# Kernel tuning notes

Measured on AMD Instinct MI355X. Metric: run time of the kernel, lower is better.

The kernel has to match this reference:

```python
import jax, jax.numpy as jnp
import numpy as np

H = 4                      # num_heads hard-coded in SDHGNN
NAMES = ["self", "cross", "self", "cross"]
POOL_SIZES = [2, 2, 2, 2]
MIN_NGHS = 128             # minium_nghs
EPS = 1e-3                 # InstanceNorm1d eps


def _pw(x, W, b):
    # pointwise Conv1d(kernel=1): [B, Cin, N] -> [B, Cout, N]
    return jnp.einsum('oi,bin->bon', W, x) + b[None, :, None]


def _instnorm(x):
    # InstanceNorm1d (no affine): normalize over N per (B, C)
    m = jnp.mean(x, axis=2, keepdims=True)
    v = jnp.mean((x - m) ** 2, axis=2, keepdims=True)
    return (x - m) * jax.lax.rsqrt(v + EPS)


def _attn_prop(x, src, p):
    # SharedAttentionalPropagation (sharing_attention=False):
    # MultiHeadedAttention + concat + MLP residual update.
    Wq, bq, Wk, bk, Wv, bv, Wm, bm, W1, b1, W2, b2 = p
    B, D, N = x.shape
    dh = D // H
    q = _pw(x, Wq, bq).reshape(B, dh, H, N)
    k = _pw(src, Wk, bk).reshape(B, dh, H, -1)
    v = _pw(src, Wv, bv).reshape(B, dh, H, -1)
    scores = jnp.einsum('bdhn,bdhm->bhnm', q, k) * (dh ** -0.5)
    prob = jax.nn.softmax(scores, axis=-1)                     # [B,H,N,M]
    msg = jnp.einsum('bhnm,bdhm->bdhn', prob, v).reshape(B, D, N)
    msg = _pw(msg, Wm, bm)
    y = jnp.concatenate([x, msg], axis=1)                      # [B,2D,N]
    h = jax.nn.relu(_instnorm(_pw(y, W1, b1)))
    return x + _pw(h, W2, b2), prob


def _gather(x, idx):
    # x: [B,D,N], idx: [B,K] -> [B,D,K]
    return jnp.take_along_axis(
        x, jnp.broadcast_to(idx[:, None, :], (x.shape[0], x.shape[1], idx.shape[1])), axis=2)


def _pool(prob, idx, pool_size):
    # pooling_by_prob (4-D prob branch): mean over heads, sum over queries,
    # top-k by importance, sorted indices, gather global indexes.
    K = idx.shape[1]
    p = prob.mean(axis=1).sum(axis=1)                          # [B,K]
    k = min(max(K // pool_size, MIN_NGHS), K)
    _, top = jax.lax.top_k(p, k)
    top = jnp.sort(top, axis=1)
    return jnp.take_along_axis(idx, top, axis=1)


def setup_inputs() -> dict:
    key = jax.random.key(0)
    B, D, N, L = 2, 128, 2048, 4
    ks = jax.random.split(key, 16)
    s = lambda fan: 1.0 / np.sqrt(fan)
    inp = {
        'x0': jax.random.normal(ks[0], (B, D, N), jnp.float32),
        'x1': jax.random.normal(ks[1], (B, D, N), jnp.float32),
        'Wq': jax.random.normal(ks[2], (L, D, D), jnp.float32) * s(D),
        'bq': jax.random.normal(ks[3], (L, D), jnp.float32) * 0.01,
        'Wk': jax.random.normal(ks[4], (L, D, D), jnp.float32) * s(D),
        'bk': jax.random.normal(ks[5], (L, D), jnp.float32) * 0.01,
        'Wv': jax.random.normal(ks[6], (L, D, D), jnp.float32) * s(D),
        'bv': jax.random.normal(ks[7], (L, D), jnp.float32) * 0.01,
        'Wm': jax.random.normal(ks[8], (L, D, D), jnp.float32) * s(D),
        'bm': jax.random.normal(ks[9], (L, D), jnp.float32) * 0.01,
        'W1': jax.random.normal(ks[10], (L, 2 * D, 2 * D), jnp.float32) * s(2 * D),
        'b1': jax.random.normal(ks[11], (L, 2 * D), jnp.float32) * 0.01,
        'W2': jax.random.normal(ks[12], (L, D, 2 * D), jnp.float32) * s(2 * D),
        'b2': jnp.zeros((L, D), jnp.float32),  # nn.init.constant_(mlp[-1].bias, 0)
    }
    return inp


def reference(x0, x1, Wq, bq, Wk, bk, Wv, bv, Wm, bm, W1, b1, W2, b2):
    B, D, N = x0.shape
    idx0 = jnp.broadcast_to(jnp.arange(N, dtype=jnp.int32)[None], (B, N))
    idx1 = idx0
    for l, (name, ps) in enumerate(zip(NAMES, POOL_SIZES)):
        p = (Wq[l], bq[l], Wk[l], bk[l], Wv[l], bv[l],
             Wm[l], bm[l], W1[l], b1[l], W2[l], b2[l])
        if name == 'self':
            s0, s1 = _gather(x0, idx0), _gather(x1, idx1)
        else:
            s0, s1 = _gather(x1, idx1), _gather(x0, idx0)
        x0, prob0 = _attn_prop(x0, s0, p)
        x1, prob1 = _attn_prop(x1, s1, p)
        if name == 'self':
            idx0 = _pool(prob0, idx0, ps)
            idx1 = _pool(prob1, idx1, ps)
        else:
            idx1 = _pool(prob0, idx1, ps)
            idx0 = _pool(prob1, idx0, ps)
    return jnp.stack([x0, x1], axis=0)   # [2, B, D, N]
```

## Files before the change

kernel.cpp:

```cpp
#include <hip/hip_runtime.h>
#include <cstdint>
#include <cstddef>


#define NB 2
#define ND 128
#define NH 4
#define NN 2048
#define ND2 256
#define DN (ND*NN)
#define BDN (NB*DN)
#define QK_SCALE 0.17677669529663687f
#define IN_EPS 1e-3f

typedef unsigned short u16;
typedef __attribute__((ext_vector_type(8))) short short8;
typedef __attribute__((ext_vector_type(4))) float f32x4;

__device__ __forceinline__ u16 f2bf(float f) {
    unsigned u = __float_as_uint(f);
    return (u16)((u + 0x7fffu + ((u >> 16) & 1u)) >> 16);
}
__device__ __forceinline__ float bf2f(u16 h) {
    return __uint_as_float(((unsigned)h) << 16);
}

__global__ __launch_bounds__(256) void init_kernel(
    const float* __restrict__ x0in, const float* __restrict__ x1in,
    float* __restrict__ out, int* __restrict__ idx0, int* __restrict__ idx1)
{
    int tid = blockIdx.x * 256 + threadIdx.x;
    const float4* a = (const float4*)x0in;
    const float4* b = (const float4*)x1in;
    float4* o = (float4*)out;
    o[tid] = a[tid];
    o[BDN/4 + tid] = b[tid];
    if (tid < NB*NN) {
        int v = tid & (NN-1);
        idx0[tid] = v;
        idx1[tid] = v;
    }
}

__global__ __launch_bounds__(256) void wrepack2_kernel(
    const float* __restrict__ Wq, const float* __restrict__ Wk,
    const float* __restrict__ Wv, const float* __restrict__ Wm,
    const float* __restrict__ W1, const float* __restrict__ W2,
    const float* __restrict__ bq, const float* __restrict__ bk,
    const float* __restrict__ bv,
    u16* __restrict__ whi, u16* __restrict__ wlo,
    float* __restrict__ bqp, float* __restrict__ bkp, float* __restrict__ bvp)
{
    int e = blockIdx.x * 256 + threadIdx.x;
    if (e < 655360) {
        int l = e / 163840, r = e - l*163840;
        float v;
        if (r < 49152) {
            int m = r >> 14;
            int rr = r & 16383;
            int o = rr >> 7, c = rr & 127;
            int so = (o & 31)*4 + (o >> 5);
            const float* W = (m == 0) ? Wq : ((m == 1) ? Wk : Wv);
            v = W[l*16384 + so*128 + c];
        } else if (r < 65536) {
            int rr = r - 49152;
            int o = rr >> 7, c = rr & 127;
            int sc = (c & 31)*4 + (c >> 5);
            v = Wm[l*16384 + o*128 + sc];
        } else if (r < 131072) v = W1[l*65536 + r - 65536];
        else                   v = W2[l*32768 + r - 131072];
        u16 hb = f2bf(v);
        whi[e] = hb;
        wlo[e] = f2bf(v - bf2f(hb));
    } else if (e < 656896) {
        int eb = e - 655360;
        int l = eb / 384, rr = eb % 384;
        int which = rr >> 7, o = rr & 127;
        int so = (o & 31)*4 + (o >> 5);
        float v = (which == 0 ? bq : (which == 1 ? bk : bv))[l*128 + so];
        (which == 0 ? bqp : (which == 1 ? bkp : bvp))[l*128 + o] = v;
    }
}

__global__ __launch_bounds__(256) void repack_xh_kernel(
    const float* __restrict__ in, u16* __restrict__ ohi, u16* __restrict__ olo)
{
    __shared__ float tile[32][68];
    int z = blockIdx.y >> 2, cg = blockIdx.y & 3;
    int n0 = blockIdx.x * 64;
    int t = threadIdx.x;
    {
        int i = t >> 3, nc = (t & 7) * 8;
        const float* src = &in[((size_t)z*128 + cg*32 + i)*NN + n0 + nc];
        float4 a = *(const float4*)src;
        float4 b = *(const float4*)(src + 4);
        tile[i][nc+0]=a.x; tile[i][nc+1]=a.y; tile[i][nc+2]=a.z; tile[i][nc+3]=a.w;
        tile[i][nc+4]=b.x; tile[i][nc+5]=b.y; tile[i][nc+6]=b.z; tile[i][nc+7]=b.w;
    }
    __syncthreads();
    int n = t >> 2, c8 = (t & 3) * 8;
    short8 hi, lo;
    #pragma unroll
    for (int j = 0; j < 8; ++j) {
        float v = tile[c8 + j][n];
        u16 h = f2bf(v);
        hi[j] = (short)h;
        lo[j] = (short)f2bf(v - bf2f(h));
    }
    size_t ob = ((size_t)z*NN + n0 + n)*128 + cg*32 + c8;
    *(short8*)&ohi[ob] = hi;
    *(short8*)&olo[ob] = lo;
}

__device__ __forceinline__ void gcore(
    u16* As0, u16* As1, u16* Bs0, u16* Bs1,
    const u16* __restrict__ Whi, const u16* __restrict__ Wlo, int o0, int Cin,
    const u16* __restrict__ B1hi, const u16* __restrict__ B1lo, int s1,
    const u16* __restrict__ B2hi, const u16* __restrict__ B2lo, int s2, int split,
    size_t brow, int n0, const int* __restrict__ idxp, int t, f32x4 acc[2][2])
{
    const int lane = t & 63, w = t >> 6;
    const int l15 = lane & 15, quad = lane >> 4;
    const int wr = (w & 1)*32, wc = (w >> 1)*32;
    const int ao = t >> 2, ak = (t & 3)*8;
    int grow = n0 + ao;
    if (idxp) grow = idxp[grow];
    for (int kc = 0; kc < Cin; kc += 32) {
        {
            size_t wa = (size_t)(o0 + ao)*Cin + kc + ak;
            *(short8*)&As0[ao*40 + ak] = *(const short8*)&Whi[wa];
            *(short8*)&As1[ao*40 + ak] = *(const short8*)&Wlo[wa];
        }
        {
            int c = kc + ak;
            const u16 *ph, *pl;
            size_t off;
            if (c < split) { ph = B1hi; pl = B1lo; off = (brow + grow)*s1 + c; }
            else { ph = B2hi; pl = B2lo; off = (brow + grow)*s2 + (c - split); }
            *(short8*)&Bs0[ao*40 + ak] = *(const short8*)&ph[off];
            *(short8*)&Bs1[ao*40 + ak] = *(const short8*)&pl[off];
        }
        __syncthreads();
        short8 Ah[2], Al[2], Bh[2], Bl[2];
        #pragma unroll
        for (int a = 0; a < 2; ++a) {
            Ah[a] = *(const short8*)&As0[(wr + a*16 + l15)*40 + quad*8];
            Al[a] = *(const short8*)&As1[(wr + a*16 + l15)*40 + quad*8];
        }
        #pragma unroll
        for (int c = 0; c < 2; ++c) {
            Bh[c] = *(const short8*)&Bs0[(wc + c*16 + l15)*40 + quad*8];
            Bl[c] = *(const short8*)&Bs1[(wc + c*16 + l15)*40 + quad*8];
        }
        #pragma unroll
        for (int a = 0; a < 2; ++a)
            #pragma unroll
            for (int c = 0; c < 2; ++c) {
                acc[a][c] = __builtin_amdgcn_mfma_f32_16x16x32_bf16(Ah[a], Bl[c], acc[a][c], 0,0,0);
                acc[a][c] = __builtin_amdgcn_mfma_f32_16x16x32_bf16(Al[a], Bh[c], acc[a][c], 0,0,0);
                acc[a][c] = __builtin_amdgcn_mfma_f32_16x16x32_bf16(Ah[a], Bh[c], acc[a][c], 0,0,0);
            }
        __syncthreads();
    }
}

__global__ __launch_bounds__(256) void qkv_kernel(
    const u16* __restrict__ Whi, const u16* __restrict__ Wlo,
    const float* __restrict__ bqp, const float* __restrict__ bkp,
    const float* __restrict__ bvp,
    const u16* __restrict__ xphi, const u16* __restrict__ xplo,
    const int* __restrict__ idx0, const int* __restrict__ idx1,
    int cross, int M,
    u16* __restrict__ qthi, u16* __restrict__ qtlo,
    u16* __restrict__ kthi, u16* __restrict__ ktlo,
    u16* __restrict__ vthi, float* __restrict__ p)
{
    __shared__ u16 gsm[10240];
    u16* As0 = gsm;  u16* As1 = gsm + 2560;
    u16* Bs0 = gsm + 5120; u16* Bs1 = gsm + 7680;
    float* tb = (float*)gsm;

    const int z = blockIdx.z;
    const int bx = blockIdx.x;
    const int t = threadIdx.x;
    const int lane = t & 63, w = t >> 6;
    const int l15 = lane & 15, quad = lane >> 4;
    const int wr = (w & 1)*32, wc = (w >> 1)*32;

    int role, o0, n0, nCols;
    const u16 *Wbh, *Wbl;
    const float* bias;
    if (bx < 64) {
        role = 0; o0 = (bx & 1)*64; n0 = (bx >> 1)*64; nCols = NN;
        Wbh = Whi; Wbl = Wlo; bias = bqp;
        if (t < 32) p[(size_t)z*NN + bx*32 + t] = 0.f;
    } else {
        int e = bx - 64;
        int kt = M >> 6;
        int ct = e % kt, rt = e / kt;
        n0 = ct*64; nCols = M;
        if (rt < 2) { role = 1; o0 = rt*64; Wbh = Whi+16384; Wbl = Wlo+16384; bias = bkp; }
        else        { role = 2; o0 = (rt-2)*64; Wbh = Whi+32768; Wbl = Wlo+32768; bias = bvp; }
    }
    size_t brow = (size_t)z * NN;
    const int* idxp = nullptr;
    if (role != 0) {
        int ss = cross ? 1 - (z >> 1) : (z >> 1);
        brow = (size_t)(ss*2 + (z & 1)) * NN;
        idxp = (ss ? idx1 : idx0) + (z & 1)*NN;
    }

    f32x4 acc[2][2];
    #pragma unroll
    for (int a = 0; a < 2; ++a)
        #pragma unroll
        for (int c = 0; c < 2; ++c) acc[a][c] = (f32x4){0.f,0.f,0.f,0.f};

    gcore(As0, As1, Bs0, Bs1, Wbh, Wbl, o0, 128,
          xphi, xplo, 128, xphi, xplo, 128, 128, brow, n0, idxp, t, acc);

    if (role == 2) {
        #pragma unroll
        for (int a = 0; a < 2; ++a)
            #pragma unroll
            for (int c = 0; c < 2; ++c)
                #pragma unroll
                for (int r = 0; r < 4; ++r) {
                    int row = o0 + wr + a*16 + quad*4 + r;
                    int m = n0 + wc + c*16 + l15;
                    float v = acc[a][c][r] + bias[row];
                    vthi[((size_t)(z*4 + (row>>5))*32 + (row&31))*(size_t)M + m] = f2bf(v);
                }
    } else {
        float scale = role ? 1.f : QK_SCALE;
        #pragma unroll
        for (int a = 0; a < 2; ++a)
            #pragma unroll
            for (int c = 0; c < 2; ++c)
                #pragma unroll
                for (int r = 0; r < 4; ++r) {
                    int rl = wr + a*16 + quad*4 + r;
                    tb[rl*66 + wc + c*16 + l15] = acc[a][c][r] + bias[o0 + rl];
                }
        __syncthreads();
        u16* ohi = role ? kthi : qthi;
        u16* olo = role ? ktlo : qtlo;
        int n = t >> 2, rb = (t & 3)*16;
        #pragma unroll
        for (int g = 0; g < 2; ++g) {
            short8 hi, lo;
            #pragma unroll
            for (int j = 0; j < 8; ++j) {
                float v = tb[(rb + g*8 + j)*66 + n] * scale;
                u16 hb = f2bf(v);
                hi[j] = (short)hb;
                lo[j] = (short)f2bf(v - bf2f(hb));
            }
            int rowg = o0 + rb + g*8;
            size_t ob = ((size_t)(z*4 + (rowg >> 5))*nCols + n0 + n)*32 + (rowg & 31);
            *(short8*)&ohi[ob] = hi;
            *(short8*)&olo[ob] = lo;
        }
    }
}

__global__ __launch_bounds__(512) void attn4_kernel(
    const u16* __restrict__ qthi, const u16* __restrict__ qtlo,
    const u16* __restrict__ kthi, const u16* __restrict__ ktlo,
    const u16* __restrict__ vthi, int M,
    u16* __restrict__ msghi, u16* __restrict__ msglo, float* __restrict__ p)
{
    __shared__ u16 kv[14592];
    __shared__ u16 Pw[64][146];
    __shared__ float pcol[2048];
    __shared__ float redm[4][64], redl[4][64];
    __shared__ float rowM[64], rowIV[64];

    u16* ks0 = kv;
    u16* ks1 = kv + 5120;
    u16* vs  = kv + 10240;
    float* obuf = (float*)kv;

    const int t = threadIdx.x;
    const int lane = t & 63, wave = t >> 6;
    const int l15 = lane & 15, quad = lane >> 4;
    const int qp = wave & 1, mh = wave >> 1;
    const int h = blockIdx.y, z = blockIdx.z;
    const int zh = z*4 + h;
    const int n0 = blockIdx.x * 64;

    for (int i = t; i < M; i += 512) pcol[i] = 0.f;

    short8 qBh[2], qBl[2];
    #pragma unroll
    for (int qt = 0; qt < 2; ++qt) {
        size_t qb = ((size_t)zh*NN + n0 + qp*32 + qt*16 + l15)*32 + quad*8;
        qBh[qt] = *(const short8*)&qthi[qb];
        qBl[qt] = *(const short8*)&qtlo[qb];
    }

    const int nch = M >> 7;
    const int sr = t >> 2, sc8 = (t & 3)*8;
    const int vr = t >> 4, vc8 = (t & 15)*8;

    float rm[2] = {-1e30f, -1e30f}, rl[2] = {0.f, 0.f};

    for (int ch = 0; ch < nch; ++ch) {
        const int m0 = ch << 7;
        {
            size_t gk = ((size_t)zh*M + m0 + sr)*32 + sc8;
            *(short8*)&ks0[sr*40 + sc8] = *(const short8*)&kthi[gk];
            *(short8*)&ks1[sr*40 + sc8] = *(const short8*)&ktlo[gk];
        }
        __syncthreads();
        #pragma unroll
        for (int qt = 0; qt < 2; ++qt)
            #pragma unroll
            for (int mt = 0; mt < 2; ++mt) {
                int mrow = mh*32 + mt*16 + l15;
                short8 kh = *(const short8*)&ks0[mrow*40 + quad*8];
                short8 kl = *(const short8*)&ks1[mrow*40 + quad*8];
                f32x4 a = {0.f,0.f,0.f,0.f};
                a = __builtin_amdgcn_mfma_f32_16x16x32_bf16(kh, qBl[qt], a, 0,0,0);
                a = __builtin_amdgcn_mfma_f32_16x16x32_bf16(kl, qBh[qt], a, 0,0,0);
                a = __builtin_amdgcn_mfma_f32_16x16x32_bf16(kh, qBh[qt], a, 0,0,0);
                float bm = fmaxf(fmaxf(a[0],a[1]), fmaxf(a[2],a[3]));
                float bs = __expf(a[0]-bm)+__expf(a[1]-bm)+__expf(a[2]-bm)+__expf(a[3]-bm);
                if (bm > rm[qt]) { rl[qt] = rl[qt]*__expf(rm[qt]-bm) + bs; rm[qt] = bm; }
                else rl[qt] += bs*__expf(bm - rm[qt]);
            }
        __syncthreads();
    }

    #pragma unroll
    for (int qt = 0; qt < 2; ++qt) {
        #pragma unroll
        for (int off = 16; off <= 32; off <<= 1) {
            float om = __shfl_xor(rm[qt], off);
            float ol = __shfl_xor(rl[qt], off);
            float nm = fmaxf(rm[qt], om);
            rl[qt] = rl[qt]*__expf(rm[qt]-nm) + ol*__expf(om-nm);
            rm[qt] = nm;
        }
        if (quad == 0) {
            redm[mh][qp*32 + qt*16 + l15] = rm[qt];
            redl[mh][qp*32 + qt*16 + l15] = rl[qt];
        }
    }
    __syncthreads();
    if (t < 64) {
        float m = redm[0][t], l = redl[0][t];
        #pragma unroll
        for (int w2 = 1; w2 < 4; ++w2) {
            float om = redm[w2][t];
            float nm = fmaxf(m, om);
            l = l*__expf(m - nm) + redl[w2][t]*__expf(om - nm);
            m = nm;
        }
        rowM[t] = m;
        rowIV[t] = 1.f / l;
    }
    __syncthreads();
    float myRM[2], myRIV[2];
    #pragma unroll
    for (int qt = 0; qt < 2; ++qt) {
        myRM[qt]  = rowM[qp*32 + qt*16 + l15];
        myRIV[qt] = rowIV[qp*32 + qt*16 + l15];
    }

    f32x4 oa[2][2];
    #pragma unroll
    for (int qt = 0; qt < 2; ++qt)
        #pragma unroll
        for (int dt = 0; dt < 2; ++dt) oa[qt][dt] = (f32x4){0.f,0.f,0.f,0.f};

    for (int ch = 0; ch < nch; ++ch) {
        const int m0 = ch << 7;
        {
            size_t gk = ((size_t)zh*M + m0 + sr)*32 + sc8;
            *(short8*)&ks0[sr*40 + sc8] = *(const short8*)&kthi[gk];
            *(short8*)&ks1[sr*40 + sc8] = *(const short8*)&ktlo[gk];
            *(short8*)&vs[vr*136 + vc8] =
                *(const short8*)&vthi[((size_t)zh*32 + vr)*M + m0 + vc8];
        }
        __syncthreads();

        float pr[2][2][4];
        #pragma unroll
        for (int qt = 0; qt < 2; ++qt)
            #pragma unroll
            for (int mt = 0; mt < 2; ++mt) {
                int mrow = mh*32 + mt*16 + l15;
                short8 kh = *(const short8*)&ks0[mrow*40 + quad*8];
                short8 kl = *(const short8*)&ks1[mrow*40 + quad*8];
                f32x4 a = {0.f,0.f,0.f,0.f};
                a = __builtin_amdgcn_mfma_f32_16x16x32_bf16(kh, qBl[qt], a, 0,0,0);
                a = __builtin_amdgcn_mfma_f32_16x16x32_bf16(kl, qBh[qt], a, 0,0,0);
                a = __builtin_amdgcn_mfma_f32_16x16x32_bf16(kh, qBh[qt], a, 0,0,0);
                #pragma unroll
                for (int r = 0; r < 4; ++r)
                    pr[qt][mt][r] = __expf(a[r] - myRM[qt]) * myRIV[qt];
            }

        #pragma unroll
        for (int mt = 0; mt < 2; ++mt)
            #pragma unroll
            for (int r = 0; r < 4; ++r) {
                float ps = pr[0][mt][r] + pr[1][mt][r];
                ps += __shfl_xor(ps, 1);
                ps += __shfl_xor(ps, 2);
                ps += __shfl_xor(ps, 4);
                ps += __shfl_xor(ps, 8);
                if (l15 == 0)
                    atomicAdd(&pcol[m0 + mh*32 + mt*16 + quad*4 + r], ps);
            }

        #pragma unroll
        for (int qt = 0; qt < 2; ++qt) {
            int qrow = qp*32 + qt*16 + l15;
            #pragma unroll
            for (int mt = 0; mt < 2; ++mt) {
                u16 h0 = f2bf(pr[qt][mt][0]), h1 = f2bf(pr[qt][mt][1]);
                u16 h2 = f2bf(pr[qt][mt][2]), h3 = f2bf(pr[qt][mt][3]);
                uint2 hv;
                hv.x = (unsigned)h0 | ((unsigned)h1 << 16);
                hv.y = (unsigned)h2 | ((unsigned)h3 << 16);
                *(uint2*)&Pw[qrow][mh*36 + mt*16 + quad*4] = hv;
            }
        }

        #pragma unroll
        for (int qt = 0; qt < 2; ++qt) {
            int qrow = qp*32 + qt*16 + l15;
            short8 pAh = *(const short8*)&Pw[qrow][mh*36 + quad*8];
            #pragma unroll
            for (int dt = 0; dt < 2; ++dt) {
                short8 vh = *(const short8*)&vs[(dt*16 + l15)*136 + mh*32 + quad*8];
                oa[qt][dt] = __builtin_amdgcn_mfma_f32_16x16x32_bf16(pAh, vh, oa[qt][dt], 0,0,0);
            }
        }
        __syncthreads();
    }

    if (mh > 0) {
        #pragma unroll
        for (int qt = 0; qt < 2; ++qt)
            #pragma unroll
            for (int dt = 0; dt < 2; ++dt)
                #pragma unroll
                for (int r = 0; r < 4; ++r) {
                    int q = qp*32 + qt*16 + quad*4 + r;
                    obuf[((mh-1)*64 + q)*32 + dt*16 + l15] = oa[qt][dt][r];
                }
    }
    __syncthreads();
    if (mh == 0) {
        #pragma unroll
        for (int qt = 0; qt < 2; ++qt)
            #pragma unroll
            for (int dt = 0; dt < 2; ++dt)
                #pragma unroll
                for (int r = 0; r < 4; ++r) {
                    int q = qp*32 + qt*16 + quad*4 + r;
                    float v = oa[qt][dt][r];
                    #pragma unroll
                    for (int w2 = 0; w2 < 3; ++w2)
                        v += obuf[(w2*64 + q)*32 + dt*16 + l15];
                    obuf[q*32 + dt*16 + l15] = v;
                }
    }
    __syncthreads();
    {
        int tt = t & 255;
        int n = tt >> 2, i8 = (tt & 3)*8;
        short8 o8;
        if (t < 256) {
            #pragma unroll
            for (int j = 0; j < 8; ++j) o8[j] = (short)f2bf(obuf[n*32 + i8 + j]);
            *(short8*)&msghi[((size_t)z*NN + n0 + n)*128 + h*32 + i8] = o8;
        } else {
            #pragma unroll
            for (int j = 0; j < 8; ++j) {
                float v = obuf[n*32 + i8 + j];
                u16 hb = f2bf(v);
                o8[j] = (short)f2bf(v - bf2f(hb));
            }
            *(short8*)&msglo[((size_t)z*NN + n0 + n)*128 + h*32 + i8] = o8;
        }
    }
    for (int i = t; i < M; i += 512)
        atomicAdd(&p[(size_t)z*NN + i], pcol[i]*0.25f);
}

__global__ __launch_bounds__(256) void wm_kernel(
    const u16* __restrict__ Wmh, const u16* __restrict__ Wml,
    const float* __restrict__ bm,
    const u16* __restrict__ msghi, const u16* __restrict__ msglo,
    u16* __restrict__ m2hi, u16* __restrict__ m2lo,
    float* __restrict__ gsum, float* __restrict__ gsq)
{
    __shared__ u16 gsm[10240];
    u16* As0 = gsm;  u16* As1 = gsm + 2560;
    u16* Bs0 = gsm + 5120; u16* Bs1 = gsm + 7680;
    float* tb = (float*)gsm;

    const int z = blockIdx.z, o0 = blockIdx.y*64, n0 = blockIdx.x*64;
    const int t = threadIdx.x;
    const int lane = t & 63, w = t >> 6;
    const int l15 = lane & 15, quad = lane >> 4;
    const int wr = (w & 1)*32, wc = (w >> 1)*32;

    if (blockIdx.x == 0 && blockIdx.y == 0) {
        gsum[z*256 + t] = 0.f;
        gsq[z*256 + t] = 0.f;
    }

    f32x4 acc[2][2];
    #pragma unroll
    for (int a = 0; a < 2; ++a)
        #pragma unroll
        for (int c = 0; c < 2; ++c) acc[a][c] = (f32x4){0.f,0.f,0.f,0.f};
    gcore(As0, As1, Bs0, Bs1, Wmh, Wml, o0, 128,
          msghi, msglo, 128, msghi, msglo, 128, 128,
          (size_t)z*NN, n0, nullptr, t, acc);

    #pragma unroll
    for (int a = 0; a < 2; ++a)
        #pragma unroll
        for (int c = 0; c < 2; ++c)
            #pragma unroll
            for (int r = 0; r < 4; ++r) {
                int rl = wr + a*16 + quad*4 + r;
                tb[rl*66 + wc + c*16 + l15] = acc[a][c][r] + bm[o0 + rl];
            }
    __syncthreads();
    int n = t >> 2, rb = (t & 3)*16;
    #pragma unroll
    for (int g = 0; g < 2; ++g) {
        short8 hi, lo;
        #pragma unroll
        for (int j = 0; j < 8; ++j) {
            float v = tb[(rb + g*8 + j)*66 + n];
            u16 hb = f2bf(v);
            hi[j] = (short)hb;
            lo[j] = (short)f2bf(v - bf2f(hb));
        }
        size_t ob = ((size_t)z*NN + n0 + n)*128 + o0 + rb + g*8;
        *(short8*)&m2hi[ob] = hi;
        *(short8*)&m2lo[ob] = lo;
    }
}

__global__ __launch_bounds__(256) void w1_kernel(
    const u16* __restrict__ W1h, const u16* __restrict__ W1l,
    const float* __restrict__ b1,
    const u16* __restrict__ xphi, const u16* __restrict__ xplo,
    const u16* __restrict__ m2hi, const u16* __restrict__ m2lo,
    float* __restrict__ zf, float* __restrict__ gsum, float* __restrict__ gsq)
{
    __shared__ u16 gsm[10240];
    u16* As0 = gsm;  u16* As1 = gsm + 2560;
    u16* Bs0 = gsm + 5120; u16* Bs1 = gsm + 7680;

    const int z = blockIdx.z, o0 = blockIdx.y*64, n0 = blockIdx.x*64;
    const int t = threadIdx.x;
    const int lane = t & 63, w = t >> 6;
    const int l15 = lane & 15, quad = lane >> 4;
    const int wr = (w & 1)*32, wc = (w >> 1)*32;

    f32x4 acc[2][2];
    #pragma unroll
    for (int a = 0; a < 2; ++a)
        #pragma unroll
        for (int c = 0; c < 2; ++c) acc[a][c] = (f32x4){0.f,0.f,0.f,0.f};
    gcore(As0, As1, Bs0, Bs1, W1h, W1l, o0, 256,
          xphi, xplo, 128, m2hi, m2lo, 128, 128,
          (size_t)z*NN, n0, nullptr, t, acc);

    float ssum[2][4], ssq[2][4];
    #pragma unroll
    for (int a = 0; a < 2; ++a)
        #pragma unroll
        for (int r = 0; r < 4; ++r) { ssum[a][r] = 0.f; ssq[a][r] = 0.f; }
    #pragma unroll
    for (int a = 0; a < 2; ++a)
        #pragma unroll
        for (int c = 0; c < 2; ++c)
            #pragma unroll
            for (int r = 0; r < 4; ++r) {
                int row = o0 + wr + a*16 + quad*4 + r;
                int n = n0 + wc + c*16 + l15;
                float v = acc[a][c][r] + b1[row];
                zf[((size_t)z*256 + row)*NN + n] = v;
                ssum[a][r] += v;
                ssq[a][r] = fmaf(v, v, ssq[a][r]);
            }
    #pragma unroll
    for (int a = 0; a < 2; ++a)
        #pragma unroll
        for (int r = 0; r < 4; ++r) {
            float s = ssum[a][r], q2 = ssq[a][r];
            #pragma unroll
            for (int o = 1; o < 16; o <<= 1) {
                s  += __shfl_xor(s, o);
                q2 += __shfl_xor(q2, o);
            }
            if (l15 == 0) {
                int row = o0 + wr + a*16 + quad*4 + r;
                atomicAdd(&gsum[z*256 + row], s);
                atomicAdd(&gsq[z*256 + row], q2);
            }
        }
}

__global__ __launch_bounds__(256) void hrepack_kernel(
    const float* __restrict__ zf, const float* __restrict__ gsum,
    const float* __restrict__ gsq, u16* __restrict__ hhi, u16* __restrict__ hlo)
{
    __shared__ float tile[32][68];
    int z = blockIdx.y >> 3, cg = blockIdx.y & 7;
    int n0 = blockIdx.x * 64;
    int t = threadIdx.x;
    {
        int i = t >> 3, nc = (t & 7) * 8;
        int c = cg*32 + i;
        float mean = gsum[z*256 + c] * (1.f/NN);
        float var = gsq[z*256 + c] * (1.f/NN) - mean*mean;
        float iv = rsqrtf(var + IN_EPS);
        const float* src = &zf[((size_t)z*256 + c)*NN + n0 + nc];
        float4 a = *(const float4*)src;
        float4 b = *(const float4*)(src + 4);
        float vv[8] = {a.x,a.y,a.z,a.w,b.x,b.y,b.z,b.w};
        #pragma unroll
        for (int j = 0; j < 8; ++j) {
            float v = (vv[j] - mean) * iv;
            tile[i][nc + j] = v > 0.f ? v : 0.f;
        }
    }
    __syncthreads();
    int n = t >> 2, c8 = (t & 3) * 8;
    short8 hi, lo;
    #pragma unroll
    for (int j = 0; j < 8; ++j) {
        float v = tile[c8 + j][n];
        u16 hb = f2bf(v);
        hi[j] = (short)hb;
        lo[j] = (short)f2bf(v - bf2f(hb));
    }
    size_t ob = ((size_t)z*NN + n0 + n)*256 + cg*32 + c8;
    *(short8*)&hhi[ob] = hi;
    *(short8*)&hlo[ob] = lo;
}

__global__ __launch_bounds__(256) void w2_kernel(
    const u16* __restrict__ W2h, const u16* __restrict__ W2l,
    const float* __restrict__ b2,
    const u16* __restrict__ hhi, const u16* __restrict__ hlo,
    float* __restrict__ out, u16* __restrict__ xphi, u16* __restrict__ xplo,
    int writeplanes)
{
    __shared__ u16 gsm[10240];
    u16* As0 = gsm;  u16* As1 = gsm + 2560;
    u16* Bs0 = gsm + 5120; u16* Bs1 = gsm + 7680;
    float* tb = (float*)gsm;

    const int z = blockIdx.z, o0 = blockIdx.y*64, n0 = blockIdx.x*64;
    const int t = threadIdx.x;
    const int lane = t & 63, w = t >> 6;
    const int l15 = lane & 15, quad = lane >> 4;
    const int wr = (w & 1)*32, wc = (w >> 1)*32;

    f32x4 acc[2][2];
    #pragma unroll
    for (int a = 0; a < 2; ++a)
        #pragma unroll
        for (int c = 0; c < 2; ++c) acc[a][c] = (f32x4){0.f,0.f,0.f,0.f};
    gcore(As0, As1, Bs0, Bs1, W2h, W2l, o0, 256,
          hhi, hlo, 256, hhi, hlo, 256, 256,
          (size_t)z*NN, n0, nullptr, t, acc);

    #pragma unroll
    for (int a = 0; a < 2; ++a)
        #pragma unroll
        for (int c = 0; c < 2; ++c)
            #pragma unroll
            for (int r = 0; r < 4; ++r) {
                int rl = wr + a*16 + quad*4 + r;
                int rowg = o0 + rl;
                int n = n0 + wc + c*16 + l15;
                size_t oi = ((size_t)z*128 + rowg)*NN + n;
                float v = acc[a][c][r] + b2[rowg] + out[oi];
                out[oi] = v;
                tb[rl*66 + wc + c*16 + l15] = v;
            }
    __syncthreads();
    if (writeplanes) {
        int n = t >> 2, rb = (t & 3)*16;
        #pragma unroll
        for (int g = 0; g < 2; ++g) {
            short8 hi, lo;
            #pragma unroll
            for (int j = 0; j < 8; ++j) {
                float v = tb[(rb + g*8 + j)*66 + n];
                u16 hb = f2bf(v);
                hi[j] = (short)hb;
                lo[j] = (short)f2bf(v - bf2f(hb));
            }
            size_t ob = ((size_t)z*NN + n0 + n)*128 + o0 + rb + g*8;
            *(short8*)&xphi[ob] = hi;
            *(short8*)&xplo[ob] = lo;
        }
    }
}

__global__ __launch_bounds__(256) void rank_kernel(
    const float* __restrict__ p, int* __restrict__ rank, int M)
{
    int zz = blockIdx.y;
    __shared__ float pv[2048];
    for (int i = threadIdx.x; i < M; i += 256) pv[i] = p[(size_t)zz*NN + i];
    __syncthreads();
    int i = blockIdx.x * 256 + threadIdx.x;
    if (i < M) {
        float pi = pv[i];
        int r = 0;
        for (int j = 0; j < M; ++j) {
            float pj = pv[j];
            r += (pj > pi) ? 1 : ((pj == pi && j < i) ? 1 : 0);
        }
        rank[zz*NN + i] = r;
    }
}

__global__ __launch_bounds__(256) void select_kernel(
    const int* __restrict__ rank, int* __restrict__ idx0, int* __restrict__ idx1,
    int M, int k, int cross)
{
    int z = blockIdx.x;
    int st = z >> 1, b = z & 1;
    int ts = cross ? 1 - st : st;
    int* idx = (ts ? idx1 : idx0) + b * NN;
    const int* rk = rank + z * NN;
    __shared__ int sel[2048], idv[2048], sa[2048], sb[2048];
    int t = threadIdx.x;
    for (int i = t; i < M; i += 256) {
        int s = rk[i] < k ? 1 : 0;
        sel[i] = s;
        sa[i] = s;
        idv[i] = idx[i];
    }
    __syncthreads();
    int* src = sa; int* dst = sb;
    for (int off = 1; off < M; off <<= 1) {
        for (int i = t; i < M; i += 256)
            dst[i] = src[i] + (i >= off ? src[i - off] : 0);
        __syncthreads();
        int* tmp = src; src = dst; dst = tmp;
    }
    for (int i = t; i < M; i += 256)
        if (sel[i]) idx[src[i] - 1] = idv[i];
}

extern "C" void kernel_launch(void* const* d_in, const int* in_sizes, int n_in,
                              void* d_out, int out_size, void* d_ws, size_t ws_size,
                              hipStream_t stream)
{
    const float* x0in = (const float*)d_in[0];
    const float* x1in = (const float*)d_in[1];
    const float* Wq = (const float*)d_in[2];
    const float* bq = (const float*)d_in[3];
    const float* Wk = (const float*)d_in[4];
    const float* bk = (const float*)d_in[5];
    const float* Wv = (const float*)d_in[6];
    const float* bv = (const float*)d_in[7];
    const float* Wm = (const float*)d_in[8];
    const float* bm = (const float*)d_in[9];
    const float* W1 = (const float*)d_in[10];
    const float* b1 = (const float*)d_in[11];
    const float* W2 = (const float*)d_in[12];
    const float* b2 = (const float*)d_in[13];

    float* out = (float*)d_out;
    float* ws  = (float*)d_ws;

    const size_t U = 1048576;
    u16* ub   = (u16*)ws;
    u16* xphi = ub;            u16* xplo = ub + U;
    u16* qthi = ub + 2*U;      u16* qtlo = ub + 3*U;
    u16* kthi = ub + 4*U;      u16* ktlo = ub + 5*U;
    u16* vthi = ub + 6*U;
    u16* msghi = ub + 7*U;     u16* msglo = ub + 8*U;
    u16* m2hi = ub + 9*U;      u16* m2lo = ub + 10*U;
    u16* hhi  = ub + 11*U;     u16* hlo = ub + 13*U;
    u16* whi  = ub + 15*U;     u16* wlo = whi + 655360;
    float* zf = (float*)(ub + 2*U);
    float* ft = (float*)(wlo + 655360);
    float* bqp = ft;           float* bkp = ft + 512;      float* bvp = ft + 1024;
    float* gsum = ft + 1536;   float* gsq = ft + 2560;
    float* p = ft + 3584;
    int* idx0 = (int*)(p + 4*NN);
    int* idx1 = idx0 + NB*NN;
    int* rankb = idx1 + NB*NN;

    init_kernel<<<BDN/4/256, 256, 0, stream>>>(x0in, x1in, out, idx0, idx1);
    wrepack2_kernel<<<2566, 256, 0, stream>>>(Wq, Wk, Wv, Wm, W1, W2, bq, bk, bv,
                                              whi, wlo, bqp, bkp, bvp);
    repack_xh_kernel<<<dim3(32, 16), 256, 0, stream>>>(out, xphi, xplo);

    const int Ms[4] = {2048, 1024, 512, 256};
    for (int l = 0; l < 4; ++l) {
        int M = Ms[l];
        int k_new = (M/2 < 128) ? 128 : M/2;
        int cross = l & 1;
        size_t lw = (size_t)l * 163840;
        const u16* Wlh = whi + lw;  const u16* Wll = wlo + lw;

        qkv_kernel<<<dim3(64 + 4*(M/64), 1, 4), 256, 0, stream>>>(
            Wlh, Wll, bqp + l*128, bkp + l*128, bvp + l*128,
            xphi, xplo, idx0, idx1, cross, M,
            qthi, qtlo, kthi, ktlo, vthi, p);

        attn4_kernel<<<dim3(32, NH, 4), 512, 0, stream>>>(
            qthi, qtlo, kthi, ktlo, vthi, M, msghi, msglo, p);

        wm_kernel<<<dim3(32, 2, 4), 256, 0, stream>>>(
            Wlh + 49152, Wll + 49152, bm + l*128,
            msghi, msglo, m2hi, m2lo, gsum, gsq);

        w1_kernel<<<dim3(32, 4, 4), 256, 0, stream>>>(
            Wlh + 65536, Wll + 65536, b1 + l*256,
            xphi, xplo, m2hi, m2lo, zf, gsum, gsq);

        hrepack_kernel<<<dim3(32, 32), 256, 0, stream>>>(zf, gsum, gsq, hhi, hlo);

        w2_kernel<<<dim3(32, 2, 4), 256, 0, stream>>>(
            Wlh + 131072, Wll + 131072, b2 + l*128,
            hhi, hlo, out, xphi, xplo, (l < 3) ? 1 : 0);

        rank_kernel<<<dim3((M+255)/256, 4), 256, 0, stream>>>(p, rankb, M);
        select_kernel<<<4, 256, 0, stream>>>(rankb, idx0, idx1, M, k_new, cross);
    }
}
```

Baseline: 555.9 us.

## Keep attention P in registers via bpermute and use exp2 softmax

Removes the shared-memory P staging buffer in the attention kernel. Probabilities are packed to bf16 with v_cvt_pk_bf16_f32 and rearranged across lanes with ds_bpermute, and the PV MFMA runs with V as the A operand, which transposes the output layout. Softmax now uses exp2 with the log2(e) factor folded into QK_SCALE, and the 1/l normalisation is deferred to the final output write. Occupancy is raised through launch bounds. This cuts LDS traffic and ALU work but adds cross-lane permutes and a changed output-reduction layout.

Result: slower. 567.4 us (+2.1%).

```diff
diff --git a/kernel.cpp b/kernel.cpp
--- a/kernel.cpp
+++ b/kernel.cpp
@@ -10,7 +10,7 @@
 #define ND2 256
 #define DN (ND*NN)
 #define BDN (NB*DN)
-#define QK_SCALE 0.17677669529663687f
+#define QK_SCALE 0.2550348623f
 #define IN_EPS 1e-3f
 
 typedef unsigned short u16;
@@ -23,6 +23,18 @@
 }
 __device__ __forceinline__ float bf2f(u16 h) {
     return __uint_as_float(((unsigned)h) << 16);
+}
+__device__ __forceinline__ float fexp2(float x) {
+#if __has_builtin(__builtin_amdgcn_exp2f)
+    return __builtin_amdgcn_exp2f(x);
+#else
+    return exp2f(x);
+#endif
+}
+__device__ __forceinline__ unsigned cvtpk_bf16(float a, float b) {
+    unsigned r;
+    asm("v_cvt_pk_bf16_f32 %0, %1, %2" : "=v"(r) : "v"(a), "v"(b));
+    return r;
 }
 
 __global__ __launch_bounds__(256) void init_kernel(
@@ -264,14 +276,13 @@
     }
 }
 
-__global__ __launch_bounds__(512) void attn4_kernel(
+__global__ __launch_bounds__(512, 6) void attn4_kernel(
     const u16* __restrict__ qthi, const u16* __restrict__ qtlo,
     const u16* __restrict__ kthi, const u16* __restrict__ ktlo,
     const u16* __restrict__ vthi, int M,
     u16* __restrict__ msghi, u16* __restrict__ msglo, float* __restrict__ p)
 {
     __shared__ u16 kv[14592];
-    __shared__ u16 Pw[64][146];
     __shared__ float pcol[2048];
     __shared__ float redm[4][64], redl[4][64];
     __shared__ float rowM[64], rowIV[64];
@@ -325,9 +336,9 @@
                 a = __builtin_amdgcn_mfma_f32_16x16x32_bf16(kl, qBh[qt], a, 0,0,0);
                 a = __builtin_amdgcn_mfma_f32_16x16x32_bf16(kh, qBh[qt], a, 0,0,0);
                 float bm = fmaxf(fmaxf(a[0],a[1]), fmaxf(a[2],a[3]));
-                float bs = __expf(a[0]-bm)+__expf(a[1]-bm)+__expf(a[2]-bm)+__expf(a[3]-bm);
-                if (bm > rm[qt]) { rl[qt] = rl[qt]*__expf(rm[qt]-bm) + bs; rm[qt] = bm; }
-                else rl[qt] += bs*__expf(bm - rm[qt]);
+                float bs = fexp2(a[0]-bm)+fexp2(a[1]-bm)+fexp2(a[2]-bm)+fexp2(a[3]-bm);
+                if (bm > rm[qt]) { rl[qt] = rl[qt]*fexp2(rm[qt]-bm) + bs; rm[qt] = bm; }
+                else rl[qt] += bs*fexp2(bm - rm[qt]);
             }
         __syncthreads();
     }
@@ -339,7 +350,7 @@
             float om = __shfl_xor(rm[qt], off);
             float ol = __shfl_xor(rl[qt], off);
             float nm = fmaxf(rm[qt], om);
-            rl[qt] = rl[qt]*__expf(rm[qt]-nm) + ol*__expf(om-nm);
+            rl[qt] = rl[qt]*fexp2(rm[qt]-nm) + ol*fexp2(om-nm);
             rm[qt] = nm;
         }
         if (quad == 0) {
@@ -354,7 +365,7 @@
         for (int w2 = 1; w2 < 4; ++w2) {
             float om = redm[w2][t];
             float nm = fmaxf(m, om);
-            l = l*__expf(m - nm) + redl[w2][t]*__expf(om - nm);
+            l = l*fexp2(m - nm) + redl[w2][t]*fexp2(om - nm);
             m = nm;
         }
         rowM[t] = m;
@@ -373,6 +384,10 @@
     for (int qt = 0; qt < 2; ++qt)
         #pragma unroll
         for (int dt = 0; dt < 2; ++dt) oa[qt][dt] = (f32x4){0.f,0.f,0.f,0.f};
+
+    const int aA = (l15 + 32*(quad & 1))*4;
+    const int aB = aA + 64;
+    const bool mtsel = (quad >= 2);
 
     for (int ch = 0; ch < nch; ++ch) {
         const int m0 = ch << 7;
@@ -399,14 +414,14 @@
                 a = __builtin_amdgcn_mfma_f32_16x16x32_bf16(kh, qBh[qt], a, 0,0,0);
                 #pragma unroll
                 for (int r = 0; r < 4; ++r)
-                    pr[qt][mt][r] = __expf(a[r] - myRM[qt]) * myRIV[qt];
+                    pr[qt][mt][r] = fexp2(a[r] - myRM[qt]);
             }
 
         #pragma unroll
         for (int mt = 0; mt < 2; ++mt)
             #pragma unroll
             for (int r = 0; r < 4; ++r) {
-                float ps = pr[0][mt][r] + pr[1][mt][r];
+                float ps = pr[0][mt][r]*myRIV[0] + pr[1][mt][r]*myRIV[1];
                 ps += __shfl_xor(ps, 1);
                 ps += __shfl_xor(ps, 2);
                 ps += __shfl_xor(ps, 4);
@@ -415,29 +430,33 @@
                     atomicAdd(&pcol[m0 + mh*32 + mt*16 + quad*4 + r], ps);
             }
 
+        short8 vA[2];
+        #pragma unroll
+        for (int dt = 0; dt < 2; ++dt)
+            vA[dt] = *(const short8*)&vs[(dt*16 + l15)*136 + mh*32 + quad*8];
+
         #pragma unroll
         for (int qt = 0; qt < 2; ++qt) {
-            int qrow = qp*32 + qt*16 + l15;
-            #pragma unroll
-            for (int mt = 0; mt < 2; ++mt) {
-                u16 h0 = f2bf(pr[qt][mt][0]), h1 = f2bf(pr[qt][mt][1]);
-                u16 h2 = f2bf(pr[qt][mt][2]), h3 = f2bf(pr[qt][mt][3]);
-                uint2 hv;
-                hv.x = (unsigned)h0 | ((unsigned)h1 << 16);
-                hv.y = (unsigned)h2 | ((unsigned)h3 << 16);
-                *(uint2*)&Pw[qrow][mh*36 + mt*16 + quad*4] = hv;
-            }
-        }
-
-        #pragma unroll
-        for (int qt = 0; qt < 2; ++qt) {
-            int qrow = qp*32 + qt*16 + l15;
-            short8 pAh = *(const short8*)&Pw[qrow][mh*36 + quad*8];
-            #pragma unroll
-            for (int dt = 0; dt < 2; ++dt) {
-                short8 vh = *(const short8*)&vs[(dt*16 + l15)*136 + mh*32 + quad*8];
-                oa[qt][dt] = __builtin_amdgcn_mfma_f32_16x16x32_bf16(pAh, vh, oa[qt][dt], 0,0,0);
-            }
+            unsigned pk00 = cvtpk_bf16(pr[qt][0][0], pr[qt][0][1]);
+            unsigned pk01 = cvtpk_bf16(pr[qt][0][2], pr[qt][0][3]);
+            unsigned pk10 = cvtpk_bf16(pr[qt][1][0], pr[qt][1][1]);
+            unsigned pk11 = cvtpk_bf16(pr[qt][1][2], pr[qt][1][3]);
+            unsigned a0 = (unsigned)__builtin_amdgcn_ds_bpermute(aA, (int)pk00);
+            unsigned a1 = (unsigned)__builtin_amdgcn_ds_bpermute(aA, (int)pk01);
+            unsigned a2 = (unsigned)__builtin_amdgcn_ds_bpermute(aA, (int)pk10);
+            unsigned a3 = (unsigned)__builtin_amdgcn_ds_bpermute(aA, (int)pk11);
+            unsigned b0 = (unsigned)__builtin_amdgcn_ds_bpermute(aB, (int)pk00);
+            unsigned b1 = (unsigned)__builtin_amdgcn_ds_bpermute(aB, (int)pk01);
+            unsigned b2 = (unsigned)__builtin_amdgcn_ds_bpermute(aB, (int)pk10);
+            unsigned b3 = (unsigned)__builtin_amdgcn_ds_bpermute(aB, (int)pk11);
+            union { unsigned u[4]; short8 s; } fb;
+            fb.u[0] = mtsel ? a2 : a0;
+            fb.u[1] = mtsel ? a3 : a1;
+            fb.u[2] = mtsel ? b2 : b0;
+            fb.u[3] = mtsel ? b3 : b1;
+            #pragma unroll
+            for (int dt = 0; dt < 2; ++dt)
+                oa[qt][dt] = __builtin_amdgcn_mfma_f32_16x16x32_bf16(vA[dt], fb.s, oa[qt][dt], 0,0,0);
         }
         __syncthreads();
     }
@@ -449,8 +468,9 @@
             for (int dt = 0; dt < 2; ++dt)
                 #pragma unroll
                 for (int r = 0; r < 4; ++r) {
-                    int q = qp*32 + qt*16 + quad*4 + r;
-                    obuf[((mh-1)*64 + q)*32 + dt*16 + l15] = oa[qt][dt][r];
+                    int q = qp*32 + qt*16 + l15;
+                    int d = dt*16 + quad*4 + r;
+                    obuf[((mh-1)*32 + d)*66 + q] = oa[qt][dt][r];
                 }
     }
     __syncthreads();
@@ -461,12 +481,13 @@
             for (int dt = 0; dt < 2; ++dt)
                 #pragma unroll
                 for (int r = 0; r < 4; ++r) {
-                    int q = qp*32 + qt*16 + quad*4 + r;
+                    int q = qp*32 + qt*16 + l15;
+                    int d = dt*16 + quad*4 + r;
                     float v = oa[qt][dt][r];
                     #pragma unroll
                     for (int w2 = 0; w2 < 3; ++w2)
-                        v += obuf[(w2*64 + q)*32 + dt*16 + l15];
-                    obuf[q*32 + dt*16 + l15] = v;
+                        v += obuf[(w2*32 + d)*66 + q];
+                    obuf[d*66 + q] = v * myRIV[qt];
                 }
     }
     __syncthreads();
@@ -476,12 +497,12 @@
         short8 o8;
         if (t < 256) {
             #pragma unroll
-            for (int j = 0; j < 8; ++j) o8[j] = (short)f2bf(obuf[n*32 + i8 + j]);
+            for (int j = 0; j < 8; ++j) o8[j] = (short)f2bf(obuf[(i8+j)*66 + n]);
             *(short8*)&msghi[((size_t)z*NN + n0 + n)*128 + h*32 + i8] = o8;
         } else {
             #pragma unroll
             for (int j = 0; j < 8; ++j) {
-                float v = obuf[n*32 + i8 + j];
+                float v = obuf[(i8+j)*66 + n];
                 u16 hb = f2bf(v);
                 o8[j] = (short)f2bf(v - bf2f(hb));
             }
```
